# Kernel tuning notes

Hardware: AMD Instinct MI355X
Metric: run time of the kernel (lower is better)

Reference implementation:

```python
import jax, jax.numpy as jnp
import numpy as np
import math

B, S, D_MODEL, N_HEAD, D_HEAD, D_FFN = 1, 2048, 1024, 16, 64, 4096
EPS = 1e-6


def setup_inputs() -> dict:
    key = jax.random.key(0)
    ks = jax.random.split(key, 10)
    scale = 0.02
    x = jax.random.normal(ks[0], (B, S, D_MODEL), dtype=jnp.float32)
    # RoPE frequencies: freqs_cis[s, i] = exp(1j * s * theta_i), theta_i = 10000^{-2i/d_head}
    half = D_HEAD // 2
    inv_freq = 1.0 / (10000.0 ** (jnp.arange(0, half, dtype=jnp.float32) * 2.0 / D_HEAD))
    angles = jnp.arange(S, dtype=jnp.float32)[:, None] * inv_freq[None, :]  # [S, half]
    freqs_cos = jnp.cos(angles)
    freqs_sin = jnp.sin(angles)
    wq = jax.random.normal(ks[1], (D_MODEL, N_HEAD * D_HEAD), dtype=jnp.float32) * scale
    wk = jax.random.normal(ks[2], (D_MODEL, N_HEAD * D_HEAD), dtype=jnp.float32) * scale
    wv = jax.random.normal(ks[3], (D_MODEL, N_HEAD * D_HEAD), dtype=jnp.float32) * scale
    wo = jax.random.normal(ks[4], (N_HEAD * D_HEAD, D_MODEL), dtype=jnp.float32) * scale
    w1 = jax.random.normal(ks[5], (D_MODEL, D_FFN), dtype=jnp.float32) * scale
    w2 = jax.random.normal(ks[6], (D_FFN, D_MODEL), dtype=jnp.float32) * scale
    w3 = jax.random.normal(ks[7], (D_MODEL, D_FFN), dtype=jnp.float32) * scale
    attn_norm_w = jnp.ones((D_MODEL,), dtype=jnp.float32)
    ffn_norm_w = jnp.ones((D_MODEL,), dtype=jnp.float32)
    return {"x": x, "freqs_cos": freqs_cos, "freqs_sin": freqs_sin,
            "wq": wq, "wk": wk, "wv": wv, "wo": wo,
            "w1": w1, "w2": w2, "w3": w3,
            "attn_norm_w": attn_norm_w, "ffn_norm_w": ffn_norm_w}


def _rmsnorm(x, w):
    xf = x.astype(jnp.float32)
    inv = jax.lax.rsqrt(jnp.mean(xf * xf, axis=-1, keepdims=True) + EPS)
    return (xf * inv).astype(x.dtype) * w


def _rope(t, cos, sin):
    # t: [B, S, H, D]; treat last dim as interleaved (even, odd) complex pairs
    b, s, h, d = t.shape
    tr = t.astype(jnp.float32).reshape(b, s, h, d // 2, 2)
    te, to = tr[..., 0], tr[..., 1]
    c = cos[None, :, None, :]
    sn = sin[None, :, None, :]
    out = jnp.stack([te * c - to * sn, te * sn + to * c], axis=-1)
    return out.reshape(b, s, h, d).astype(t.dtype)


def reference(x, freqs_cos, freqs_sin, wq, wk, wv, wo, w1, w2, w3, attn_norm_w, ffn_norm_w):
    bsz, seqlen, _ = x.shape
    # --- attention sub-block ---
    hin = _rmsnorm(x, attn_norm_w)
    q = (hin @ wq).reshape(bsz, seqlen, N_HEAD, D_HEAD)
    k = (hin @ wk).reshape(bsz, seqlen, N_HEAD, D_HEAD)
    v = (hin @ wv).reshape(bsz, seqlen, N_HEAD, D_HEAD)
    q = _rope(q, freqs_cos, freqs_sin)
    k = _rope(k, freqs_cos, freqs_sin)
    # [B, H, S, S] scores, softmax in fp32 (no causal mask in original)
    scores = jnp.einsum('bqhd,bkhd->bhqk', q, k) / math.sqrt(D_HEAD)
    probs = jax.nn.softmax(scores.astype(jnp.float32), axis=-1).astype(q.dtype)
    attn = jnp.einsum('bhqk,bkhd->bqhd', probs, v).reshape(bsz, seqlen, N_HEAD * D_HEAD)
    h = x + attn @ wo
    # --- SwiGLU FFN sub-block ---
    f = _rmsnorm(h, ffn_norm_w)
    ffn = (jax.nn.silu(f @ w1) * (f @ w3)) @ w2
    return h + ffn
```

## Files before the change

kernel.cpp:

```cpp
#include <hip/hip_runtime.h>
#include <stdint.h>
#include <stddef.h>

using bf16x8 = __attribute__((ext_vector_type(8))) __bf16;
using f32x4  = __attribute__((ext_vector_type(4))) float;
using f32x16 = __attribute__((ext_vector_type(16))) float;

__device__ __forceinline__ float bf2f(unsigned short u) {
  union { unsigned int i; float f; } v; v.i = ((unsigned int)u) << 16; return v.f;
}
__device__ __forceinline__ unsigned short f2bf(float f) {
  union { float f; unsigned int i; } v; v.f = f;
  unsigned int r = v.i + 0x7fffu + ((v.i >> 16) & 1u);
  return (unsigned short)(r >> 16);
}
__device__ __forceinline__ unsigned short f2bf_trunc(float f) {
  union { float f; unsigned int i; } v; v.f = f;
  return (unsigned short)(v.i >> 16);
}
__device__ __forceinline__ void async16(const void* g, void* l) {
  __builtin_amdgcn_global_load_lds(
      (const __attribute__((address_space(1))) unsigned int*)g,
      (__attribute__((address_space(3))) unsigned int*)l, 16, 0, 0);
}

#define S_LEN 2048
#define DMODEL 1024
#define NHEAD 16
#define DHEAD 64
#define DFFN 4096

struct T4 {
  const float *s0, *s1, *s2, *s3;
  unsigned short *d0, *d1, *d2, *d3;
};
__global__ __launch_bounds__(256) void transpose4_k(T4 j) {
  const float* in = blockIdx.z == 0 ? j.s0 : blockIdx.z == 1 ? j.s1 : blockIdx.z == 2 ? j.s2 : j.s3;
  unsigned short* out = blockIdx.z == 0 ? j.d0 : blockIdx.z == 1 ? j.d1 : blockIdx.z == 2 ? j.d2 : j.d3;
  __shared__ unsigned short tile[32][33];
  const int tx = threadIdx.x & 31;
  const int ty = threadIdx.x >> 5;
  const int bc = blockIdx.x * 32;
  const int br = blockIdx.y * 32;
#pragma unroll
  for (int i = 0; i < 4; ++i)
    tile[ty + i * 8][tx] = f2bf(in[(size_t)(br + ty + i * 8) * 1024 + bc + tx]);
  __syncthreads();
#pragma unroll
  for (int i = 0; i < 4; ++i)
    out[(size_t)(bc + ty + i * 8) * 1024 + br + tx] = tile[tx][ty + i * 8];
}

__global__ __launch_bounds__(256) void transpose13_k(
    const float* __restrict__ w1, const float* __restrict__ w3,
    unsigned short* __restrict__ out) {
  const float* in = blockIdx.z ? w3 : w1;
  const int rb = blockIdx.z * 32;
  __shared__ unsigned short tile[32][33];
  const int tx = threadIdx.x & 31;
  const int ty = threadIdx.x >> 5;
  const int bc = blockIdx.x * 32;
  const int br = blockIdx.y * 32;
#pragma unroll
  for (int i = 0; i < 4; ++i)
    tile[ty + i * 8][tx] = f2bf(in[(size_t)(br + ty + i * 8) * 4096 + bc + tx]);
  __syncthreads();
#pragma unroll
  for (int i = 0; i < 4; ++i) {
    int c = bc + ty + i * 8;
    int dest = (c >> 5) * 64 + rb + (c & 31);
    out[(size_t)dest * 1024 + br + tx] = tile[tx][ty + i * 8];
  }
}

__global__ __launch_bounds__(256) void transpose_w2_k(
    const float* __restrict__ in, unsigned short* __restrict__ out) {
  __shared__ unsigned short tile[32][33];
  const int tx = threadIdx.x & 31;
  const int ty = threadIdx.x >> 5;
  const int bc = blockIdx.x * 32;
  const int br = blockIdx.y * 32;
#pragma unroll
  for (int i = 0; i < 4; ++i)
    tile[ty + i * 8][tx] = f2bf(in[(size_t)(br + ty + i * 8) * 1024 + bc + tx]);
  __syncthreads();
#pragma unroll
  for (int i = 0; i < 4; ++i)
    out[(size_t)(bc + ty + i * 8) * 4096 + br + tx] = tile[tx][ty + i * 8];
}

__global__ __launch_bounds__(256) void vtrans_k(
    const unsigned short* __restrict__ QKV, unsigned short* __restrict__ VtG) {
  __shared__ unsigned short tile[32][33];
  const int tx = threadIdx.x & 31;
  const int ty = threadIdx.x >> 5;
  const int bc = blockIdx.x * 32;
  const int br = blockIdx.y * 32;
#pragma unroll
  for (int i = 0; i < 4; ++i)
    tile[ty + i * 8][tx] = QKV[(size_t)(br + ty + i * 8) * 3072 + 2048 + bc + tx];
  __syncthreads();
#pragma unroll
  for (int i = 0; i < 4; ++i)
    VtG[(size_t)(bc + ty + i * 8) * 2048 + br + tx] = tile[tx][ty + i * 8];
}

__global__ __launch_bounds__(256) void rmsnorm_k(
    const float* __restrict__ X, const float* __restrict__ W,
    unsigned short* __restrict__ Y) {
  const int row = blockIdx.x;
  const int t = threadIdx.x;
  const int lane = t & 63, w = t >> 6;
  const float* x = X + (size_t)row * DMODEL;
  float xs[4];
  float s = 0.f;
#pragma unroll
  for (int i = 0; i < 4; ++i) {
    xs[i] = x[t * 4 + i];
    s += xs[i] * xs[i];
  }
#pragma unroll
  for (int m = 1; m < 64; m <<= 1) s += __shfl_xor(s, m, 64);
  __shared__ float red[4];
  if (lane == 0) red[w] = s;
  __syncthreads();
  float tot = red[0] + red[1] + red[2] + red[3];
  float inv = rsqrtf(tot * (1.0f / DMODEL) + 1e-6f);
#pragma unroll
  for (int i = 0; i < 4; ++i)
    Y[(size_t)row * DMODEL + t * 4 + i] = f2bf(xs[i] * inv * W[t * 4 + i]);
}

template <int MODE>
__global__ __launch_bounds__(256) void gemm_bt(
    const unsigned short* __restrict__ A, int lda,
    const unsigned short* __restrict__ BT,
    void* __restrict__ Cout,
    int K, int N) {
  __shared__ unsigned short As[128 * 64];
  __shared__ unsigned short Bs[128 * 64];
  const int t = threadIdx.x;
  const int lane = t & 63;
  const int w = t >> 6;
  const int qr = (w >> 1) * 64, qc = (w & 1) * 64;
  const int l31 = lane & 31, half = lane >> 5;
  const int m0 = blockIdx.y * 128, n0 = blockIdx.x * 128;

  f32x16 acc[2][2] = {};

  int srow[4], scol[4];
#pragma unroll
  for (int p = 0; p < 4; ++p) {
    int off = p * 2048 + t * 8;
    int r = off >> 6;
    srow[p] = r;
    scol[p] = (((off >> 3) & 7) ^ (r & 7)) * 8;
  }

  for (int k0 = 0; k0 < K; k0 += 64) {
    __syncthreads();
#pragma unroll
    for (int p = 0; p < 4; ++p) {
      int off = p * 2048 + t * 8;
      async16(A + (size_t)(m0 + srow[p]) * lda + (k0 + scol[p]), &As[off]);
      async16(BT + (size_t)(n0 + srow[p]) * K + (k0 + scol[p]), &Bs[off]);
    }
    __syncthreads();
#pragma unroll
    for (int ks = 0; ks < 4; ++ks) {
      const int ch = ((ks * 2 + half) ^ (l31 & 7)) * 8;
      bf16x8 a0 = *(const bf16x8*)&As[(qr + l31) * 64 + ch];
      bf16x8 a1 = *(const bf16x8*)&As[(qr + 32 + l31) * 64 + ch];
      bf16x8 b0 = *(const bf16x8*)&Bs[(qc + l31) * 64 + ch];
      bf16x8 b1 = *(const bf16x8*)&Bs[(qc + 32 + l31) * 64 + ch];
      acc[0][0] = __builtin_amdgcn_mfma_f32_32x32x16_bf16(a0, b0, acc[0][0], 0, 0, 0);
      acc[0][1] = __builtin_amdgcn_mfma_f32_32x32x16_bf16(a0, b1, acc[0][1], 0, 0, 0);
      acc[1][0] = __builtin_amdgcn_mfma_f32_32x32x16_bf16(a1, b0, acc[1][0], 0, 0, 0);
      acc[1][1] = __builtin_amdgcn_mfma_f32_32x32x16_bf16(a1, b1, acc[1][1], 0, 0, 0);
    }
  }

  if constexpr (MODE == 2) {
    unsigned short* C = (unsigned short*)Cout;
    const int ld = N >> 1;
#pragma unroll
    for (int rt = 0; rt < 2; ++rt)
#pragma unroll
      for (int reg = 0; reg < 16; ++reg) {
        int rr = m0 + qr + rt * 32 + (reg & 3) + 8 * (reg >> 2) + 4 * half;
        int cc = ((n0 + qc) >> 1) + l31;
        float a1v = acc[rt][0][reg];
        float a3v = acc[rt][1][reg];
        float f = a1v / (1.f + __expf(-a1v)) * a3v;
        C[(size_t)rr * ld + cc] = f2bf(f);
      }
  } else {
    unsigned short* C = (unsigned short*)Cout;
#pragma unroll
    for (int rt = 0; rt < 2; ++rt)
#pragma unroll
      for (int ct = 0; ct < 2; ++ct)
#pragma unroll
        for (int reg = 0; reg < 16; ++reg) {
          int rr = m0 + qr + rt * 32 + (reg & 3) + 8 * (reg >> 2) + 4 * half;
          int cc = n0 + qc + ct * 32 + l31;
          C[(size_t)rr * N + cc] = f2bf(acc[rt][ct][reg]);
        }
  }
}

struct PtrPair { float* p0; float* p1; };

__global__ __launch_bounds__(256) void gemm_bt_sk(
    const unsigned short* __restrict__ A, int lda,
    const unsigned short* __restrict__ BT,
    PtrPair parts, int Kc, int Ktot, int N) {
  __shared__ unsigned short As[64 * 64];
  __shared__ unsigned short Bs[128 * 64];
  const int t = threadIdx.x;
  const int lane = t & 63;
  const int w = t >> 6;
  const int qr = (w >> 1) * 32, qc = (w & 1) * 64;
  const int l31 = lane & 31, half = lane >> 5;
  const int m0 = blockIdx.y * 64, n0 = blockIdx.x * 128;
  const int kb = blockIdx.z * Kc;

  f32x16 acc[2] = {};

  for (int k0 = 0; k0 < Kc; k0 += 64) {
    __syncthreads();
#pragma unroll
    for (int p = 0; p < 2; ++p) {
      int off = p * 2048 + t * 8;
      int r = off >> 6;
      int sc = (((off >> 3) & 7) ^ (r & 7)) * 8;
      async16(A + (size_t)(m0 + r) * lda + (kb + k0 + sc), &As[off]);
    }
#pragma unroll
    for (int p = 0; p < 4; ++p) {
      int off = p * 2048 + t * 8;
      int r = off >> 6;
      int sc = (((off >> 3) & 7) ^ (r & 7)) * 8;
      async16(BT + (size_t)(n0 + r) * Ktot + (kb + k0 + sc), &Bs[off]);
    }
    __syncthreads();
#pragma unroll
    for (int ks = 0; ks < 4; ++ks) {
      const int ch = ((ks * 2 + half) ^ (l31 & 7)) * 8;
      bf16x8 a0 = *(const bf16x8*)&As[(qr + l31) * 64 + ch];
      bf16x8 b0 = *(const bf16x8*)&Bs[(qc + l31) * 64 + ch];
      bf16x8 b1 = *(const bf16x8*)&Bs[(qc + 32 + l31) * 64 + ch];
      acc[0] = __builtin_amdgcn_mfma_f32_32x32x16_bf16(a0, b0, acc[0], 0, 0, 0);
      acc[1] = __builtin_amdgcn_mfma_f32_32x32x16_bf16(a0, b1, acc[1], 0, 0, 0);
    }
  }

  float* C = blockIdx.z ? parts.p1 : parts.p0;
#pragma unroll
  for (int ct = 0; ct < 2; ++ct)
#pragma unroll
    for (int reg = 0; reg < 16; ++reg) {
      int rr = m0 + qr + (reg & 3) + 8 * (reg >> 2) + 4 * half;
      int cc = n0 + qc + ct * 32 + l31;
      C[(size_t)rr * N + cc] = acc[ct][reg];
    }
}

__global__ __launch_bounds__(256) void reduce2_k(
    const float4* __restrict__ P0, const float4* __restrict__ P1,
    const float4* __restrict__ R, float4* __restrict__ Out, int nvec) {
  int i = blockIdx.x * 256 + threadIdx.x;
  if (i >= nvec) return;
  float4 a = P0[i], b = P1[i], r = R[i];
  float4 o;
  o.x = a.x + b.x + r.x;
  o.y = a.y + b.y + r.y;
  o.z = a.z + b.z + r.z;
  o.w = a.w + b.w + r.w;
  Out[i] = o;
}

__global__ __launch_bounds__(256) void rope_k(
    unsigned short* __restrict__ QKV,
    const float* __restrict__ cosp,
    const float* __restrict__ sinp) {
  int idx = blockIdx.x * 256 + threadIdx.x;
  int s = idx >> 9;
  int rem = idx & 511;
  int h = rem >> 5;
  int i = rem & 31;
  float c = cosp[s * 32 + i];
  float sn = sinp[s * 32 + i];
  size_t off = (size_t)s * 3072 + h * 64 + 2 * i;
  {
    float e = bf2f(QKV[off]), o = bf2f(QKV[off + 1]);
    QKV[off] = f2bf(e * c - o * sn);
    QKV[off + 1] = f2bf(e * sn + o * c);
  }
  {
    float e = bf2f(QKV[off + 1024]), o = bf2f(QKV[off + 1025]);
    QKV[off + 1024] = f2bf((e * c - o * sn) * 0.125f);
    QKV[off + 1025] = f2bf((e * sn + o * c) * 0.125f);
  }
}

#define VPAD 132
__device__ __forceinline__ int swz(int row, int col) { return col ^ ((row & 7) * 8); }

__global__ __launch_bounds__(256) void attn_k(
    const unsigned short* __restrict__ QKV,
    const unsigned short* __restrict__ VtG,
    float* __restrict__ O0, float* __restrict__ O1,
    float* __restrict__ L) {
  const int h = blockIdx.y;
  const int qb = blockIdx.x;
  const int z = blockIdx.z;
  const int t = threadIdx.x;
  const int lane = t & 63;
  const int w = t >> 6;
  const int row16 = lane & 15, quad = lane >> 4;
  const int q0 = qb * 64 + w * 16;
  const int kbase = z * 1024;

  __shared__ unsigned short Ks[128 * 64];
  __shared__ unsigned short Vt[64 * 128];
  __shared__ unsigned short Ps[4][16 * VPAD];

  const unsigned short* Qp = QKV;
  const unsigned short* Kp = QKV + 1024;
  const unsigned short* Vg = VtG + (size_t)h * 64 * 2048;

  bf16x8 aq[2];
#pragma unroll
  for (int kk = 0; kk < 2; ++kk)
    aq[kk] = *(const bf16x8*)(Qp + (size_t)(q0 + row16) * 3072 + h * 64 + kk * 32 + quad * 8);

  f32x4 o[4] = {};
  float l_r[4] = {0.f, 0.f, 0.f, 0.f};

  bf16x8 kreg[4], vreg[4];
#pragma unroll
  for (int p = 0; p < 4; ++p) {
    int off = p * 2048 + t * 8;
    int r = off >> 6, c = off & 63;
    kreg[p] = *(const bf16x8*)(Kp + (size_t)(kbase + r) * 3072 + h * 64 + c);
    int d = off >> 7, key = off & 127;
    vreg[p] = *(const bf16x8*)(Vg + (size_t)d * 2048 + kbase + key);
  }

  for (int kb = kbase; kb < kbase + 1024; kb += 128) {
    __syncthreads();
#pragma unroll
    for (int p = 0; p < 4; ++p) {
      int off = p * 2048 + t * 8;
      int r = off >> 6, c = off & 63;
      *(bf16x8*)&Ks[r * 64 + swz(r, c)] = kreg[p];
      int d = off >> 7, key = off & 127;
      *(bf16x8*)&Vt[d * 128 + swz(d, key)] = vreg[p];
    }
    __syncthreads();
    if (kb + 128 < kbase + 1024) {
      int kb2 = kb + 128;
#pragma unroll
      for (int p = 0; p < 4; ++p) {
        int off = p * 2048 + t * 8;
        int r = off >> 6, c = off & 63;
        kreg[p] = *(const bf16x8*)(Kp + (size_t)(kb2 + r) * 3072 + h * 64 + c);
        int d = off >> 7, key = off & 127;
        vreg[p] = *(const bf16x8*)(Vg + (size_t)d * 2048 + kb2 + key);
      }
    }

    f32x4 sc[8];
#pragma unroll
    for (int tj = 0; tj < 8; ++tj) {
      int kr = tj * 16 + row16;
      bf16x8 b0 = *(const bf16x8*)&Ks[kr * 64 + swz(kr, quad * 8)];
      bf16x8 b1 = *(const bf16x8*)&Ks[kr * 64 + swz(kr, 32 + quad * 8)];
      f32x4 z4 = {};
      z4 = __builtin_amdgcn_mfma_f32_16x16x32_bf16(aq[0], b0, z4, 0, 0, 0);
      z4 = __builtin_amdgcn_mfma_f32_16x16x32_bf16(aq[1], b1, z4, 0, 0, 0);
      sc[tj] = z4;
    }

#pragma unroll
    for (int reg = 0; reg < 4; ++reg) {
      float ssum = 0.f;
#pragma unroll
      for (int tj = 0; tj < 8; ++tj) {
        float p = __expf(sc[tj][reg]);
        sc[tj][reg] = p;
        ssum += p;
      }
#pragma unroll
      for (int m = 1; m < 16; m <<= 1) ssum += __shfl_xor(ssum, m, 16);
      l_r[reg] += ssum;
    }

#pragma unroll
    for (int tj = 0; tj < 8; ++tj)
#pragma unroll
      for (int reg = 0; reg < 4; ++reg)
        Ps[w][(quad * 4 + reg) * VPAD + tj * 16 + row16] = f2bf_trunc(sc[tj][reg]);

    bf16x8 ap[4];
#pragma unroll
    for (int kk = 0; kk < 4; ++kk)
      ap[kk] = *(const bf16x8*)&Ps[w][row16 * VPAD + kk * 32 + quad * 8];
#pragma unroll
    for (int dt = 0; dt < 4; ++dt) {
      int dr = dt * 16 + row16;
#pragma unroll
      for (int kk = 0; kk < 4; ++kk) {
        bf16x8 bv = *(const bf16x8*)&Vt[dr * 128 + swz(dr, kk * 32 + quad * 8)];
        o[dt] = __builtin_amdgcn_mfma_f32_16x16x32_bf16(ap[kk], bv, o[dt], 0, 0, 0);
      }
    }
  }

  float* Op = z ? O1 : O0;
#pragma unroll
  for (int dt = 0; dt < 4; ++dt)
#pragma unroll
    for (int reg = 0; reg < 4; ++reg)
      Op[(size_t)(q0 + quad * 4 + reg) * DMODEL + h * 64 + dt * 16 + row16] = o[dt][reg];
  if (row16 == 0)
#pragma unroll
    for (int reg = 0; reg < 4; ++reg)
      L[(size_t)(h * 2 + z) * S_LEN + q0 + quad * 4 + reg] = l_r[reg];
}

__global__ __launch_bounds__(256) void attn_combine_k(
    const float4* __restrict__ O0, const float4* __restrict__ O1,
    const float* __restrict__ L, unsigned short* __restrict__ Attn) {
  int i = blockIdx.x * 256 + threadIdx.x;
  int e0 = i * 4;
  int s = e0 >> 10;
  int c = e0 & 1023;
  int h = c >> 6;
  float la = L[(size_t)(h * 2) * S_LEN + s];
  float lb = L[(size_t)(h * 2 + 1) * S_LEN + s];
  float inv = 1.f / (la + lb);
  float4 a = O0[i], b = O1[i];
  ushort4 r;
  r.x = f2bf((a.x + b.x) * inv);
  r.y = f2bf((a.y + b.y) * inv);
  r.z = f2bf((a.z + b.z) * inv);
  r.w = f2bf((a.w + b.w) * inv);
  *(ushort4*)(Attn + e0) = r;
}

extern "C" void kernel_launch(void* const* d_in, const int* in_sizes, int n_in,
                              void* d_out, int out_size, void* d_ws, size_t ws_size,
                              hipStream_t stream) {
  (void)in_sizes; (void)n_in; (void)out_size; (void)ws_size;
  const float* x    = (const float*)d_in[0];
  const float* fcos = (const float*)d_in[1];
  const float* fsin = (const float*)d_in[2];
  const float* wq   = (const float*)d_in[3];
  const float* wk   = (const float*)d_in[4];
  const float* wv   = (const float*)d_in[5];
  const float* wo   = (const float*)d_in[6];
  const float* w1   = (const float*)d_in[7];
  const float* w2   = (const float*)d_in[8];
  const float* w3   = (const float*)d_in[9];
  const float* anw  = (const float*)d_in[10];
  const float* fnw  = (const float*)d_in[11];
  float* out = (float*)d_out;
  char* ws = (char*)d_ws;

  unsigned short* WqkvT = (unsigned short*)(ws + 0);
  unsigned short* VtG   = (unsigned short*)(ws + 0);
  float*          Lbuf  = (float*)(ws + 4194304);
  unsigned short* WoT   = (unsigned short*)(ws + 6291456);
  unsigned short* QKV   = (unsigned short*)(ws + 8388608);
  unsigned short* Attn  = (unsigned short*)(ws + 20971520);
  float* Oa             = (float*)(ws + 25165824);
  float* Ob             = (float*)(ws + 37748736);
  float* P0a            = (float*)(ws + 8388608);
  float* P1a            = (float*)(ws + 25165824);
  unsigned short* F     = (unsigned short*)(ws + 0);
  float* P0b            = (float*)(ws + 16777216);
  float* P1b            = (float*)(ws + 25165824);
  unsigned short* Hin   = (unsigned short*)(ws + 33554432);
  float*          Hres  = (float*)        (ws + 37748736);
  unsigned short* W13I  = (unsigned short*)(ws + 46137344);
  unsigned short* W2T   = (unsigned short*)(ws + 62914560);

  transpose4_k<<<dim3(32, 32, 4), 256, 0, stream>>>(
      T4{wq, wk, wv, wo, WqkvT, WqkvT + 1048576, WqkvT + 2097152, WoT});
  transpose13_k<<<dim3(128, 32, 2), 256, 0, stream>>>(w1, w3, W13I);
  transpose_w2_k<<<dim3(32, 128), 256, 0, stream>>>(w2, W2T);

  rmsnorm_k<<<2048, 256, 0, stream>>>(x, anw, Hin);
  gemm_bt<0><<<dim3(24, 16), 256, 0, stream>>>(Hin, 1024, WqkvT, QKV, 1024, 3072);
  rope_k<<<4096, 256, 0, stream>>>(QKV, fcos, fsin);
  vtrans_k<<<dim3(32, 64), 256, 0, stream>>>(QKV, VtG);
  attn_k<<<dim3(32, 16, 2), 256, 0, stream>>>(QKV, VtG, Oa, Ob, Lbuf);
  attn_combine_k<<<2048, 256, 0, stream>>>((const float4*)Oa, (const float4*)Ob, Lbuf, Attn);
  gemm_bt_sk<<<dim3(8, 32, 2), 256, 0, stream>>>(Attn, 1024, WoT, PtrPair{P0a, P1a}, 512, 1024, 1024);
  reduce2_k<<<2048, 256, 0, stream>>>((const float4*)P0a, (const float4*)P1a,
                                      (const float4*)x, (float4*)Hres, 524288);

  rmsnorm_k<<<2048, 256, 0, stream>>>(Hres, fnw, Hin);
  gemm_bt<2><<<dim3(64, 16), 256, 0, stream>>>(Hin, 1024, W13I, F, 1024, 8192);
  gemm_bt_sk<<<dim3(8, 32, 2), 256, 0, stream>>>(F, 4096, W2T, PtrPair{P0b, P1b}, 2048, 4096, 1024);
  reduce2_k<<<2048, 256, 0, stream>>>((const float4*)P0b, (const float4*)P1b,
                                      (const float4*)Hres, (float4*)out, 524288);
}
```

Before: 313.8 us.

## Fuse weight transposes, RoPE into QKV GEMM, residual+RMSNorm, retile gated GEMM

Merges the three weight-transpose kernels into one launch and folds the RoPE rotation and query scaling into the QKV GEMM epilogue, using a lane shuffle to fetch the pair element. The split-K reduce and the second RMSNorm become one fused kernel. The W1/W3 gated GEMM moves to a 256x128 tile with four M sub-tiles per wave. Together these cut launches and intermediate global round-trips, at the cost of more registers and shared memory in the gated GEMM and half as many blocks for it.

```diff
diff --git a/kernel.cpp b/kernel.cpp
--- a/kernel.cpp
+++ b/kernel.cpp
@@ -30,63 +30,48 @@
 #define DHEAD 64
 #define DFFN 4096
 
-struct T4 {
-  const float *s0, *s1, *s2, *s3;
-  unsigned short *d0, *d1, *d2, *d3;
+struct TAll {
+  const float *wq, *wk, *wv, *wo, *w1, *w3, *w2;
+  unsigned short *qkvT, *woT, *w13I, *w2T;
 };
-__global__ __launch_bounds__(256) void transpose4_k(T4 j) {
-  const float* in = blockIdx.z == 0 ? j.s0 : blockIdx.z == 1 ? j.s1 : blockIdx.z == 2 ? j.s2 : j.s3;
-  unsigned short* out = blockIdx.z == 0 ? j.d0 : blockIdx.z == 1 ? j.d1 : blockIdx.z == 2 ? j.d2 : j.d3;
+__global__ __launch_bounds__(256) void transpose_all_k(TAll j) {
   __shared__ unsigned short tile[32][33];
   const int tx = threadIdx.x & 31;
   const int ty = threadIdx.x >> 5;
-  const int bc = blockIdx.x * 32;
-  const int br = blockIdx.y * 32;
+  const unsigned u = blockIdx.x;
+
+  const float* in;
+  unsigned short* out;
+  int bc, br, inC, outR, rs, rb;
+  if (u < 4096) {
+    int z = u >> 10;
+    bc = (u & 31) * 32; br = ((u >> 5) & 31) * 32;
+    in = z == 0 ? j.wq : z == 1 ? j.wk : z == 2 ? j.wv : j.wo;
+    out = z == 3 ? j.woT : j.qkvT + (size_t)z * 1048576;
+    inC = 1024; outR = 1024; rs = 32; rb = 0;
+  } else if (u < 12288) {
+    unsigned v = u - 4096;
+    int z = v >> 12;
+    bc = (v & 127) * 32; br = ((v >> 7) & 31) * 32;
+    in = z ? j.w3 : j.w1;
+    out = j.w13I;
+    inC = 4096; outR = 1024; rs = 64; rb = z * 32;
+  } else {
+    unsigned v = u - 12288;
+    bc = (v & 31) * 32; br = (v >> 5) * 32;
+    in = j.w2; out = j.w2T;
+    inC = 1024; outR = 4096; rs = 32; rb = 0;
+  }
 #pragma unroll
   for (int i = 0; i < 4; ++i)
-    tile[ty + i * 8][tx] = f2bf(in[(size_t)(br + ty + i * 8) * 1024 + bc + tx]);
-  __syncthreads();
-#pragma unroll
-  for (int i = 0; i < 4; ++i)
-    out[(size_t)(bc + ty + i * 8) * 1024 + br + tx] = tile[tx][ty + i * 8];
-}
-
-__global__ __launch_bounds__(256) void transpose13_k(
-    const float* __restrict__ w1, const float* __restrict__ w3,
-    unsigned short* __restrict__ out) {
-  const float* in = blockIdx.z ? w3 : w1;
-  const int rb = blockIdx.z * 32;
-  __shared__ unsigned short tile[32][33];
-  const int tx = threadIdx.x & 31;
-  const int ty = threadIdx.x >> 5;
-  const int bc = blockIdx.x * 32;
-  const int br = blockIdx.y * 32;
-#pragma unroll
-  for (int i = 0; i < 4; ++i)
-    tile[ty + i * 8][tx] = f2bf(in[(size_t)(br + ty + i * 8) * 4096 + bc + tx]);
+    tile[ty + i * 8][tx] = f2bf(in[(size_t)(br + ty + i * 8) * inC + bc + tx]);
   __syncthreads();
 #pragma unroll
   for (int i = 0; i < 4; ++i) {
     int c = bc + ty + i * 8;
-    int dest = (c >> 5) * 64 + rb + (c & 31);
-    out[(size_t)dest * 1024 + br + tx] = tile[tx][ty + i * 8];
-  }
-}
-
-__global__ __launch_bounds__(256) void transpose_w2_k(
-    const float* __restrict__ in, unsigned short* __restrict__ out) {
-  __shared__ unsigned short tile[32][33];
-  const int tx = threadIdx.x & 31;
-  const int ty = threadIdx.x >> 5;
-  const int bc = blockIdx.x * 32;
-  const int br = blockIdx.y * 32;
-#pragma unroll
-  for (int i = 0; i < 4; ++i)
-    tile[ty + i * 8][tx] = f2bf(in[(size_t)(br + ty + i * 8) * 1024 + bc + tx]);
-  __syncthreads();
-#pragma unroll
-  for (int i = 0; i < 4; ++i)
-    out[(size_t)(bc + ty + i * 8) * 4096 + br + tx] = tile[tx][ty + i * 8];
+    int dest = (c >> 5) * rs + rb + (c & 31);
+    out[(size_t)dest * outR + br + tx] = tile[tx][ty + i * 8];
+  }
 }
 
 __global__ __launch_bounds__(256) void vtrans_k(
@@ -131,12 +116,41 @@
     Y[(size_t)row * DMODEL + t * 4 + i] = f2bf(xs[i] * inv * W[t * 4 + i]);
 }
 
-template <int MODE>
-__global__ __launch_bounds__(256) void gemm_bt(
-    const unsigned short* __restrict__ A, int lda,
+__global__ __launch_bounds__(256) void fused_res_norm_k(
+    const float* __restrict__ P0, const float* __restrict__ P1,
+    const float* __restrict__ R, const float* __restrict__ W,
+    float* __restrict__ Hres, unsigned short* __restrict__ Hin) {
+  const int row = blockIdx.x;
+  const int t = threadIdx.x;
+  const int lane = t & 63, w = t >> 6;
+  const size_t base = (size_t)row * DMODEL;
+  float hs[4];
+  float s = 0.f;
+#pragma unroll
+  for (int i = 0; i < 4; ++i) {
+    int c = t * 4 + i;
+    float h = P0[base + c] + P1[base + c] + R[base + c];
+    hs[i] = h;
+    Hres[base + c] = h;
+    s += h * h;
+  }
+#pragma unroll
+  for (int m = 1; m < 64; m <<= 1) s += __shfl_xor(s, m, 64);
+  __shared__ float red[4];
+  if (lane == 0) red[w] = s;
+  __syncthreads();
+  float tot = red[0] + red[1] + red[2] + red[3];
+  float inv = rsqrtf(tot * (1.0f / DMODEL) + 1e-6f);
+#pragma unroll
+  for (int i = 0; i < 4; ++i)
+    Hin[base + t * 4 + i] = f2bf(hs[i] * inv * W[t * 4 + i]);
+}
+
+__global__ __launch_bounds__(256) void gemm_qkv_rope_k(
+    const unsigned short* __restrict__ A,
     const unsigned short* __restrict__ BT,
-    void* __restrict__ Cout,
-    int K, int N) {
+    unsigned short* __restrict__ C,
+    const float* __restrict__ cosp, const float* __restrict__ sinp) {
   __shared__ unsigned short As[128 * 64];
   __shared__ unsigned short Bs[128 * 64];
   const int t = threadIdx.x;
@@ -145,25 +159,19 @@
   const int qr = (w >> 1) * 64, qc = (w & 1) * 64;
   const int l31 = lane & 31, half = lane >> 5;
   const int m0 = blockIdx.y * 128, n0 = blockIdx.x * 128;
+  const int K = 1024, N = 3072;
 
   f32x16 acc[2][2] = {};
-
-  int srow[4], scol[4];
-#pragma unroll
-  for (int p = 0; p < 4; ++p) {
-    int off = p * 2048 + t * 8;
-    int r = off >> 6;
-    srow[p] = r;
-    scol[p] = (((off >> 3) & 7) ^ (r & 7)) * 8;
-  }
 
   for (int k0 = 0; k0 < K; k0 += 64) {
     __syncthreads();
 #pragma unroll
     for (int p = 0; p < 4; ++p) {
       int off = p * 2048 + t * 8;
-      async16(A + (size_t)(m0 + srow[p]) * lda + (k0 + scol[p]), &As[off]);
-      async16(BT + (size_t)(n0 + srow[p]) * K + (k0 + scol[p]), &Bs[off]);
+      int r = off >> 6;
+      int sc = (((off >> 3) & 7) ^ (r & 7)) * 8;
+      async16(A + (size_t)(m0 + r) * K + (k0 + sc), &As[off]);
+      async16(BT + (size_t)(n0 + r) * K + (k0 + sc), &Bs[off]);
     }
     __syncthreads();
 #pragma unroll
@@ -180,33 +188,93 @@
     }
   }
 
-  if constexpr (MODE == 2) {
-    unsigned short* C = (unsigned short*)Cout;
-    const int ld = N >> 1;
-#pragma unroll
-    for (int rt = 0; rt < 2; ++rt)
-#pragma unroll
-      for (int reg = 0; reg < 16; ++reg) {
-        int rr = m0 + qr + rt * 32 + (reg & 3) + 8 * (reg >> 2) + 4 * half;
-        int cc = ((n0 + qc) >> 1) + l31;
-        float a1v = acc[rt][0][reg];
-        float a3v = acc[rt][1][reg];
-        float f = a1v / (1.f + __expf(-a1v)) * a3v;
-        C[(size_t)rr * ld + cc] = f2bf(f);
-      }
-  } else {
-    unsigned short* C = (unsigned short*)Cout;
-#pragma unroll
-    for (int rt = 0; rt < 2; ++rt)
-#pragma unroll
-      for (int ct = 0; ct < 2; ++ct)
+#pragma unroll
+  for (int rt = 0; rt < 2; ++rt)
+#pragma unroll
+    for (int ct = 0; ct < 2; ++ct) {
+      const int colbase = n0 + qc + ct * 32;
+      const int cc = colbase + l31;
+      if (colbase < 2048) {
+        const float scale = colbase < 1024 ? 1.0f : 0.125f;
+        const int i = (cc & 63) >> 1;
 #pragma unroll
         for (int reg = 0; reg < 16; ++reg) {
           int rr = m0 + qr + rt * 32 + (reg & 3) + 8 * (reg >> 2) + 4 * half;
-          int cc = n0 + qc + ct * 32 + l31;
+          float v = acc[rt][ct][reg];
+          float vp = __shfl_xor(v, 1, 64);
+          float c = cosp[rr * 32 + i];
+          float sn = sinp[rr * 32 + i];
+          float outv = (l31 & 1) ? (vp * sn + v * c) : (v * c - vp * sn);
+          C[(size_t)rr * N + cc] = f2bf(outv * scale);
+        }
+      } else {
+#pragma unroll
+        for (int reg = 0; reg < 16; ++reg) {
+          int rr = m0 + qr + rt * 32 + (reg & 3) + 8 * (reg >> 2) + 4 * half;
           C[(size_t)rr * N + cc] = f2bf(acc[rt][ct][reg]);
         }
-  }
+      }
+    }
+}
+
+__global__ __launch_bounds__(256) void gemm_gated_k(
+    const unsigned short* __restrict__ A,
+    const unsigned short* __restrict__ BT,
+    unsigned short* __restrict__ C) {
+  __shared__ unsigned short As[256 * 64];
+  __shared__ unsigned short Bs[128 * 64];
+  const int t = threadIdx.x;
+  const int lane = t & 63;
+  const int w = t >> 6;
+  const int wm = w >> 1, wn = w & 1;
+  const int l31 = lane & 31, half = lane >> 5;
+  const int m0 = blockIdx.y * 256, n0 = blockIdx.x * 128;
+  const int K = 1024;
+
+  f32x16 acc[4][2] = {};
+
+  for (int k0 = 0; k0 < K; k0 += 64) {
+    __syncthreads();
+#pragma unroll
+    for (int p = 0; p < 8; ++p) {
+      int off = p * 2048 + t * 8;
+      int r = off >> 6;
+      int sc = (((off >> 3) & 7) ^ (r & 7)) * 8;
+      async16(A + (size_t)(m0 + r) * K + (k0 + sc), &As[off]);
+    }
+#pragma unroll
+    for (int p = 0; p < 4; ++p) {
+      int off = p * 2048 + t * 8;
+      int r = off >> 6;
+      int sc = (((off >> 3) & 7) ^ (r & 7)) * 8;
+      async16(BT + (size_t)(n0 + r) * K + (k0 + sc), &Bs[off]);
+    }
+    __syncthreads();
+#pragma unroll
+    for (int ks = 0; ks < 4; ++ks) {
+      const int ch = ((ks * 2 + half) ^ (l31 & 7)) * 8;
+      bf16x8 b0 = *(const bf16x8*)&Bs[(wn * 64 + l31) * 64 + ch];
+      bf16x8 b1 = *(const bf16x8*)&Bs[(wn * 64 + 32 + l31) * 64 + ch];
+#pragma unroll
+      for (int mt = 0; mt < 4; ++mt) {
+        bf16x8 a = *(const bf16x8*)&As[(wm * 128 + mt * 32 + l31) * 64 + ch];
+        acc[mt][0] = __builtin_amdgcn_mfma_f32_32x32x16_bf16(a, b0, acc[mt][0], 0, 0, 0);
+        acc[mt][1] = __builtin_amdgcn_mfma_f32_32x32x16_bf16(a, b1, acc[mt][1], 0, 0, 0);
+      }
+    }
+  }
+
+  const int cc = ((n0 + wn * 64) >> 1) + l31;
+#pragma unroll
+  for (int mt = 0; mt < 4; ++mt)
+#pragma unroll
+    for (int reg = 0; reg < 16; ++reg) {
+      int rr = m0 + wm * 128 + mt * 32 + (reg & 3) + 8 * (reg >> 2) + 4 * half;
+      float g1 = acc[mt][0][reg];
+      float g3 = acc[mt][1][reg];
+      float f = g1 / (1.f + __expf(-g1)) * g3;
+      C[(size_t)rr * 4096 + cc] = f2bf(f);
+    }
 }
 
 struct PtrPair { float* p0; float* p1; };
@@ -278,30 +346,6 @@
   o.z = a.z + b.z + r.z;
   o.w = a.w + b.w + r.w;
   Out[i] = o;
-}
-
-__global__ __launch_bounds__(256) void rope_k(
-    unsigned short* __restrict__ QKV,
-    const float* __restrict__ cosp,
-    const float* __restrict__ sinp) {
-  int idx = blockIdx.x * 256 + threadIdx.x;
-  int s = idx >> 9;
-  int rem = idx & 511;
-  int h = rem >> 5;
-  int i = rem & 31;
-  float c = cosp[s * 32 + i];
-  float sn = sinp[s * 32 + i];
-  size_t off = (size_t)s * 3072 + h * 64 + 2 * i;
-  {
-    float e = bf2f(QKV[off]), o = bf2f(QKV[off + 1]);
-    QKV[off] = f2bf(e * c - o * sn);
-    QKV[off + 1] = f2bf(e * sn + o * c);
-  }
-  {
-    float e = bf2f(QKV[off + 1024]), o = bf2f(QKV[off + 1025]);
-    QKV[off + 1024] = f2bf((e * c - o * sn) * 0.125f);
-    QKV[off + 1025] = f2bf((e * sn + o * c) * 0.125f);
-  }
 }
 
 #define VPAD 132
@@ -487,23 +531,18 @@
   unsigned short* W13I  = (unsigned short*)(ws + 46137344);
   unsigned short* W2T   = (unsigned short*)(ws + 62914560);
 
-  transpose4_k<<<dim3(32, 32, 4), 256, 0, stream>>>(
-      T4{wq, wk, wv, wo, WqkvT, WqkvT + 1048576, WqkvT + 2097152, WoT});
-  transpose13_k<<<dim3(128, 32, 2), 256, 0, stream>>>(w1, w3, W13I);
-  transpose_w2_k<<<dim3(32, 128), 256, 0, stream>>>(w2, W2T);
+  transpose_all_k<<<16384, 256, 0, stream>>>(
+      TAll{wq, wk, wv, wo, w1, w3, w2, WqkvT, WoT, W13I, W2T});
 
   rmsnorm_k<<<2048, 256, 0, stream>>>(x, anw, Hin);
-  gemm_bt<0><<<dim3(24, 16), 256, 0, stream>>>(Hin, 1024, WqkvT, QKV, 1024, 3072);
-  rope_k<<<4096, 256, 0, stream>>>(QKV, fcos, fsin);
+  gemm_qkv_rope_k<<<dim3(24, 16), 256, 0, stream>>>(Hin, WqkvT, QKV, fcos, fsin);
   vtrans_k<<<dim3(32, 64), 256, 0, stream>>>(QKV, VtG);
   attn_k<<<dim3(32, 16, 2), 256, 0, stream>>>(QKV, VtG, Oa, Ob, Lbuf);
   attn_combine_k<<<2048, 256, 0, stream>>>((const float4*)Oa, (const float4*)Ob, Lbuf, Attn);
   gemm_bt_sk<<<dim3(8, 32, 2), 256, 0, stream>>>(Attn, 1024, WoT, PtrPair{P0a, P1a}, 512, 1024, 1024);
-  reduce2_k<<<2048, 256, 0, stream>>>((const float4*)P0a, (const float4*)P1a,
-                                      (const float4*)x, (float4*)Hres, 524288);
-
-  rmsnorm_k<<<2048, 256, 0, stream>>>(Hres, fnw, Hin);
-  gemm_bt<2><<<dim3(64, 16), 256, 0, stream>>>(Hin, 1024, W13I, F, 1024, 8192);
+  fused_res_norm_k<<<2048, 256, 0, stream>>>(P0a, P1a, x, fnw, Hres, Hin);
+
+  gemm_gated_k<<<dim3(64, 8), 256, 0, stream>>>(Hin, W13I, F);
   gemm_bt_sk<<<dim3(8, 32, 2), 256, 0, stream>>>(F, 4096, W2T, PtrPair{P0b, P1b}, 2048, 4096, 1024);
   reduce2_k<<<2048, 256, 0, stream>>>((const float4*)P0b, (const float4*)P1b,
                                       (const float4*)Hres, (float4*)out, 524288);
```

Result: no change. 316.2 us (+0.7%).
